# Optimization experiments

Measured on AMD Instinct MI355X. Metric: run time of the kernel, lower is better.

Reference implementation:

```python
import jax, jax.numpy as jnp
import numpy as np

B, T, D, S = 2048, 1024, 32, 2  # batch, n_times, input_dim, state_dim


def setup_inputs() -> dict:
    key = jax.random.key(0)
    k1, k2, k3 = jax.random.split(key, 3)
    init_states = jax.random.normal(k1, (B, S), dtype=jnp.float32)
    z = jax.random.normal(k2, (B, T, D), dtype=jnp.float32)
    # Linear(input_dim + state_dim -> state_dim, bias=False); torch layout (out, in)
    W = jax.random.normal(k3, (S, S + D), dtype=jnp.float32) * 0.01
    W = W.at[0, 0].set(1.01).at[1, 1].set(1.0)  # matches torch __init__ overrides
    return {"init_states": init_states, "z": z, "W": W}


def reference(init_states, z, W):
    # cur_input = concat([state, z_t]); split W into state and input blocks.
    Ws = W[:, :S]   # (S, S) recurrent block
    Wz = W[:, S:]   # (S, D) input block
    # Loop runs over i in [0, T-2]; preds = [init] + T-1 updates -> (B, T, S)
    zt = jnp.swapaxes(z[:, :-1, :], 0, 1)  # (T-1, B, D)

    def step(state, z_i):
        new = state @ Ws.T + z_i @ Wz.T  # final_activation='none'
        return new, new

    _, ys = jax.lax.scan(step, init_states, zt)  # ys: (T-1, B, S)
    preds = jnp.concatenate([init_states[None], ys], axis=0)  # (T, B, S)
    return jnp.swapaxes(preds, 0, 1)  # (B, T, S)
```

## Files before the change

### kernel.cpp

```cpp
#include <hip/hip_runtime.h>


#define BB 2048
#define TT 1024
#define DD 32

__global__ __launch_bounds__(256, 8)
void ar_decoder_kernel(const float* __restrict__ init_states,
                       const float* __restrict__ z,
                       const float* __restrict__ W,
                       float* __restrict__ out)
{
    __shared__ float2 vbuf[1056];
    __shared__ float2 finals[32];
    __shared__ float2 carry[32];
    __shared__ float4 apow[32];

    const int tid = threadIdx.x;
    const int b   = blockIdx.x;
    const int j   = tid & 7;
    const int q   = tid >> 3;

    const float A00 = W[0],  A01 = W[1];
    const float A10 = W[34], A11 = W[35];

    const float w00 = W[2  + 4*j + 0], w01 = W[2  + 4*j + 1];
    const float w02 = W[2  + 4*j + 2], w03 = W[2  + 4*j + 3];
    const float w10 = W[36 + 4*j + 0], w11 = W[36 + 4*j + 1];
    const float w12 = W[36 + 4*j + 2], w13 = W[36 + 4*j + 3];

    const float4* zb = reinterpret_cast<const float4*>(z + (size_t)b * TT * DD);
    #pragma unroll 4
    for (int m = 0; m < 32; ++m) {
        const int r = 32 * m + q;
        if (r < TT - 1) {
            const float4 zv = zb[r * 8 + j];
            float p0 = zv.x*w00 + zv.y*w01 + zv.z*w02 + zv.w*w03;
            float p1 = zv.x*w10 + zv.y*w11 + zv.z*w12 + zv.w*w13;
            p0 += __shfl_xor(p0, 1, 8);  p1 += __shfl_xor(p1, 1, 8);
            p0 += __shfl_xor(p0, 2, 8);  p1 += __shfl_xor(p1, 2, 8);
            p0 += __shfl_xor(p0, 4, 8);  p1 += __shfl_xor(p1, 4, 8);
            if (j == 0) vbuf[r + (r >> 5)] = make_float2(p0, p1);
        }
    }
    __syncthreads();

    if (tid < 32) {
        const int c  = tid;
        const int n  = (c == 31) ? 31 : 32;
        float s0 = 0.f, s1 = 0.f;
        for (int k = 0; k < n; ++k) {
            const int p = 33 * c + k;
            const float2 v = vbuf[p];
            const float ns0 = fmaf(A00, s0, fmaf(A01, s1, v.x));
            const float ns1 = fmaf(A10, s0, fmaf(A11, s1, v.y));
            s0 = ns0; s1 = ns1;
            vbuf[p] = make_float2(s0, s1);
        }
        finals[c] = make_float2(s0, s1);
        float m00 = A00, m01 = A01, m10 = A10, m11 = A11;
        for (int k = 0; k < c; ++k) {
            const float t00 = A00*m00 + A01*m10;
            const float t01 = A00*m01 + A01*m11;
            const float t10 = A10*m00 + A11*m10;
            const float t11 = A10*m01 + A11*m11;
            m00 = t00; m01 = t01; m10 = t10; m11 = t11;
        }
        apow[c] = make_float4(m00, m01, m10, m11);
    }
    __syncthreads();

    if (tid == 0) {
        float c0 = init_states[2 * b], c1 = init_states[2 * b + 1];
        out[(size_t)b * TT * 2 + 0] = c0;
        out[(size_t)b * TT * 2 + 1] = c1;
        carry[0] = make_float2(c0, c1);
        const float4 A32 = apow[31];
        for (int c = 0; c < 31; ++c) {
            const float2 f = finals[c];
            const float n0 = fmaf(A32.x, c0, fmaf(A32.y, c1, f.x));
            const float n1 = fmaf(A32.z, c0, fmaf(A32.w, c1, f.y));
            c0 = n0; c1 = n1;
            carry[c + 1] = make_float2(c0, c1);
        }
    }
    __syncthreads();

    const float4 M = apow[tid & 31];
    float2* outb = reinterpret_cast<float2*>(out + (size_t)b * TT * 2);
    #pragma unroll
    for (int k = 0; k < 4; ++k) {
        const int t = tid + 1 + 256 * k;
        if (t < TT) {
            const int r = t - 1;
            const int c = r >> 5;
            const float2 l  = vbuf[r + (r >> 5)];
            const float2 cr = carry[c];
            const float o0 = fmaf(M.x, cr.x, fmaf(M.y, cr.y, l.x));
            const float o1 = fmaf(M.z, cr.x, fmaf(M.w, cr.y, l.y));
            outb[t] = make_float2(o0, o1);
        }
    }
}

extern "C" void kernel_launch(void* const* d_in, const int* in_sizes, int n_in,
                              void* d_out, int out_size, void* d_ws, size_t ws_size,
                              hipStream_t stream) {
    const float* init = (const float*)d_in[0];
    const float* z    = (const float*)d_in[1];
    const float* W    = (const float*)d_in[2];
    float*       o    = (float*)d_out;
    ar_decoder_kernel<<<BB, 256, 0, stream>>>(init, z, W, o);
}
```

Baseline: 370.4 us.

## Replace serial carry chain with warp-parallel scan and split chunk/power work

The 31-step serial carry propagation done by a single thread becomes a 32-lane Hillis-Steele scan over affine (matrix, vector) pairs using shuffles. The matrix-power computation moves to a second group of 32 threads so it runs alongside the chunk-local recurrences. The z-projection loop is peeled so its main body has no bounds check, and it uses nontemporal loads with a larger unroll. The occupancy hint in launch_bounds is dropped. The parallel scan reassociates the floating-point products, so the carries can differ slightly in the last bits from the sequential order.

```diff
diff --git a/kernel.cpp b/kernel.cpp
--- a/kernel.cpp
+++ b/kernel.cpp
@@ -5,14 +5,15 @@
 #define TT 1024
 #define DD 32
 
-__global__ __launch_bounds__(256, 8)
+typedef float fx4 __attribute__((ext_vector_type(4)));
+
+__global__ __launch_bounds__(256)
 void ar_decoder_kernel(const float* __restrict__ init_states,
                        const float* __restrict__ z,
                        const float* __restrict__ W,
                        float* __restrict__ out)
 {
     __shared__ float2 vbuf[1056];
-    __shared__ float2 finals[32];
     __shared__ float2 carry[32];
     __shared__ float4 apow[32];
 
@@ -23,18 +24,29 @@
 
     const float A00 = W[0],  A01 = W[1];
     const float A10 = W[34], A11 = W[35];
+    const float i0 = init_states[2 * b], i1 = init_states[2 * b + 1];
 
     const float w00 = W[2  + 4*j + 0], w01 = W[2  + 4*j + 1];
     const float w02 = W[2  + 4*j + 2], w03 = W[2  + 4*j + 3];
     const float w10 = W[36 + 4*j + 0], w11 = W[36 + 4*j + 1];
     const float w12 = W[36 + 4*j + 2], w13 = W[36 + 4*j + 3];
 
-    const float4* zb = reinterpret_cast<const float4*>(z + (size_t)b * TT * DD);
-    #pragma unroll 4
-    for (int m = 0; m < 32; ++m) {
+    const fx4* zb = reinterpret_cast<const fx4*>(z + (size_t)b * TT * DD);
+    #pragma unroll 8
+    for (int m = 0; m < 31; ++m) {
         const int r = 32 * m + q;
-        if (r < TT - 1) {
-            const float4 zv = zb[r * 8 + j];
+        const fx4 zv = __builtin_nontemporal_load(&zb[r * 8 + j]);
+        float p0 = zv.x*w00 + zv.y*w01 + zv.z*w02 + zv.w*w03;
+        float p1 = zv.x*w10 + zv.y*w11 + zv.z*w12 + zv.w*w13;
+        p0 += __shfl_xor(p0, 1, 8);  p1 += __shfl_xor(p1, 1, 8);
+        p0 += __shfl_xor(p0, 2, 8);  p1 += __shfl_xor(p1, 2, 8);
+        p0 += __shfl_xor(p0, 4, 8);  p1 += __shfl_xor(p1, 4, 8);
+        if (j == 0) vbuf[r + (r >> 5)] = make_float2(p0, p1);
+    }
+    {
+        const int r = 32 * 31 + q;
+        if (q < 31) {
+            const fx4 zv = __builtin_nontemporal_load(&zb[r * 8 + j]);
             float p0 = zv.x*w00 + zv.y*w01 + zv.z*w02 + zv.w*w03;
             float p1 = zv.x*w10 + zv.y*w11 + zv.z*w12 + zv.w*w13;
             p0 += __shfl_xor(p0, 1, 8);  p1 += __shfl_xor(p1, 1, 8);
@@ -45,9 +57,10 @@
     }
     __syncthreads();
 
+    float f0 = 0.f, f1 = 0.f;
     if (tid < 32) {
-        const int c  = tid;
-        const int n  = (c == 31) ? 31 : 32;
+        const int c = tid;
+        const int n = (c == 31) ? 31 : 32;
         float s0 = 0.f, s1 = 0.f;
         for (int k = 0; k < n; ++k) {
             const int p = 33 * c + k;
@@ -57,7 +70,9 @@
             s0 = ns0; s1 = ns1;
             vbuf[p] = make_float2(s0, s1);
         }
-        finals[c] = make_float2(s0, s1);
+        f0 = s0; f1 = s1;
+    } else if (tid < 64) {
+        const int c = tid - 32;
         float m00 = A00, m01 = A01, m10 = A10, m11 = A11;
         for (int k = 0; k < c; ++k) {
             const float t00 = A00*m00 + A01*m10;
@@ -70,19 +85,37 @@
     }
     __syncthreads();
 
-    if (tid == 0) {
-        float c0 = init_states[2 * b], c1 = init_states[2 * b + 1];
-        out[(size_t)b * TT * 2 + 0] = c0;
-        out[(size_t)b * TT * 2 + 1] = c1;
-        carry[0] = make_float2(c0, c1);
+    if (tid < 32) {
+        const int c = tid;
         const float4 A32 = apow[31];
-        for (int c = 0; c < 31; ++c) {
-            const float2 f = finals[c];
-            const float n0 = fmaf(A32.x, c0, fmaf(A32.y, c1, f.x));
-            const float n1 = fmaf(A32.z, c0, fmaf(A32.w, c1, f.y));
-            c0 = n0; c1 = n1;
-            carry[c + 1] = make_float2(c0, c1);
+        float P00 = A32.x, P01 = A32.y, P10 = A32.z, P11 = A32.w;
+        float g0 = f0, g1 = f1;
+        #pragma unroll
+        for (int d = 1; d < 32; d <<= 1) {
+            const float q00 = __shfl_up(P00, d, 32);
+            const float q01 = __shfl_up(P01, d, 32);
+            const float q10 = __shfl_up(P10, d, 32);
+            const float q11 = __shfl_up(P11, d, 32);
+            const float h0  = __shfl_up(g0,  d, 32);
+            const float h1  = __shfl_up(g1,  d, 32);
+            if (c >= d) {
+                const float n00 = P00*q00 + P01*q10;
+                const float n01 = P00*q01 + P01*q11;
+                const float n10 = P10*q00 + P11*q10;
+                const float n11 = P10*q01 + P11*q11;
+                g0 = fmaf(P00, h0, fmaf(P01, h1, g0));
+                g1 = fmaf(P10, h0, fmaf(P11, h1, g1));
+                P00 = n00; P01 = n01; P10 = n10; P11 = n11;
+            }
         }
+        if (c == 0) {
+            carry[0] = make_float2(i0, i1);
+            out[(size_t)b * TT * 2 + 0] = i0;
+            out[(size_t)b * TT * 2 + 1] = i1;
+        }
+        if (c <= 30)
+            carry[c + 1] = make_float2(fmaf(P00, i0, fmaf(P01, i1, g0)),
+                                       fmaf(P10, i0, fmaf(P11, i1, g1)));
     }
     __syncthreads();
 
@@ -93,9 +126,8 @@
         const int t = tid + 1 + 256 * k;
         if (t < TT) {
             const int r = t - 1;
-            const int c = r >> 5;
             const float2 l  = vbuf[r + (r >> 5)];
-            const float2 cr = carry[c];
+            const float2 cr = carry[r >> 5];
             const float o0 = fmaf(M.x, cr.x, fmaf(M.y, cr.y, l.x));
             const float o1 = fmaf(M.z, cr.x, fmaf(M.w, cr.y, l.y));
             outb[t] = make_float2(o0, o1);
```

Result: faster. 343.0 us (-7.4%).
